# Kernel tuning notes

Measured on AMD Instinct MI355X. Metric: run time of the kernel, lower is better.

Reference implementation:

```python
import jax, jax.numpy as jnp
import numpy as np

DIM_V = 512
NUM_HEADS = 8
LN_EPS = 1e-5


def _layernorm(x):
    # LayerNorm over last dim, no affine (simplified_layer_norm=True)
    mu = jnp.mean(x, axis=-1, keepdims=True)
    var = jnp.mean(jnp.square(x - mu), axis=-1, keepdims=True)
    return (x - mu) * jax.lax.rsqrt(var + LN_EPS)


def setup_inputs() -> dict:
    key = jax.random.key(0)
    ks = jax.random.split(key, 12)
    B, Nq, Nk, dQ, dK, dV = 16, 1024, 1024, 512, 512, DIM_V
    s = 0.02
    return {
        "Q": jax.random.normal(ks[0], (B, Nq, dQ), jnp.float32),
        "K": jax.random.normal(ks[1], (B, Nk, dK), jnp.float32),
        "Wq": jax.random.normal(ks[2], (dQ, dV), jnp.float32) * s,
        "bq": jnp.zeros((dV,), jnp.float32),
        "Wk": jax.random.normal(ks[3], (dK, dV), jnp.float32) * s,
        "bk": jnp.zeros((dV,), jnp.float32),
        "Wv": jax.random.normal(ks[4], (dK, dV), jnp.float32) * s,
        "bv": jnp.zeros((dV,), jnp.float32),
        "Wo": jax.random.normal(ks[5], (dV, dV), jnp.float32) * s,
        "bo": jnp.zeros((dV,), jnp.float32),
    }


def reference(Q, K, Wq, bq, Wk, bk, Wv, bv, Wo, bo):
    H = NUM_HEADS
    dh = DIM_V // H
    q = Q @ Wq + bq            # [B, Nq, dV]
    k = K @ Wk + bk            # [B, Nk, dV]
    v = K @ Wv + bv            # [B, Nk, dV]
    B, Nq, _ = q.shape
    Nk = k.shape[1]
    qh = q.reshape(B, Nq, H, dh)
    kh = k.reshape(B, Nk, H, dh)
    vh = v.reshape(B, Nk, H, dh)
    # NOTE: faithful to source — scale by sqrt(dim_V), not sqrt(head_dim)
    scores = jnp.einsum('bqhd,bkhd->bhqk', qh, kh) / jnp.sqrt(jnp.asarray(DIM_V, q.dtype))
    A = jax.nn.softmax(scores, axis=-1)                    # [B, H, Nq, Nk]
    attn = jnp.einsum('bhqk,bkhd->bqhd', A, vh).reshape(B, Nq, DIM_V)
    O = q + attn               # residual with projected Q
    O = _layernorm(O)          # ln0 (no affine)
    O = O + jax.nn.gelu(O @ Wo + bo, approximate=False)
    O = _layernorm(O)          # ln1 (no affine)
    return O
```

## Files before the change

### kernel.cpp

```cpp
#include <hip/hip_runtime.h>
#include <hip/hip_bf16.h>
#include <math.h>

typedef __bf16 bf16;
typedef __bf16 bf16x8 __attribute__((ext_vector_type(8)));
typedef float  f32x4  __attribute__((ext_vector_type(4)));

#define MFMA16(a,b,c) __builtin_amdgcn_mfma_f32_16x16x32_bf16((a),(b),(c),0,0,0)
#define ATT_SCALE 0.0441941738241592f

__device__ __forceinline__ void async16p(const void* g, void* l) {
    __builtin_amdgcn_global_load_lds((const __attribute__((address_space(1))) void*)g,
                                     (__attribute__((address_space(3))) void*)l,
                                     16, 0, 0);
}

__global__ __launch_bounds__(256) void prep_w_kernel(
    const float* __restrict__ Wq, const float* __restrict__ Wk,
    const float* __restrict__ Wv, const float* __restrict__ Wo,
    bf16* __restrict__ WqT, bf16* __restrict__ WkT,
    bf16* __restrict__ WvT, bf16* __restrict__ WoT)
{
    __shared__ float tile[32][33];
    const int bx = blockIdx.x;
    const float* W; bf16* T;
    switch (bx >> 8) {
      case 0: W=Wq; T=WqT; break;
      case 1: W=Wk; T=WkT; break;
      case 2: W=Wv; T=WvT; break;
      default: W=Wo; T=WoT; break;
    }
    const int rest = bx & 255;
    const int k0 = (rest & 15) * 32, n0 = (rest >> 4) * 32;
    const int tx = threadIdx.x & 31, ty = threadIdx.x >> 5;
    #pragma unroll
    for (int i=0;i<32;i+=8)
        tile[ty+i][tx] = W[(size_t)(k0+ty+i)*512 + n0+tx];
    __syncthreads();
    #pragma unroll
    for (int i=0;i<32;i+=8)
        T[(size_t)(n0+ty+i)*512 + k0+tx] = (bf16)tile[tx][ty+i];
}

__global__ __launch_bounds__(256, 3) void gemm_qkv_kernel(
    const float* __restrict__ Qf, const float* __restrict__ Kf,
    const bf16* __restrict__ WqT, const bf16* __restrict__ WkT,
    const bf16* __restrict__ WvT,
    const float* __restrict__ bq, const float* __restrict__ bk,
    const float* __restrict__ bv,
    bf16* __restrict__ qbb, bf16* __restrict__ kbb, bf16* __restrict__ vT)
{
    __shared__ __align__(16) char smem[49152];
    float* As32 = (float*)smem;
    bf16*  Bs   = (bf16*)(smem + 32768);
    bf16*  Lt   = (bf16*)smem;

    const int z = blockIdx.z;
    const float* A  = (z == 0) ? Qf  : Kf;
    const bf16*  BT = (z == 0) ? WqT : (z == 1) ? WkT : WvT;
    const float* bb = (z == 0) ? bq  : (z == 1) ? bk  : bv;

    const int m0 = blockIdx.x * 128, n0 = blockIdx.y * 128;
    const int tid = threadIdx.x;
    const int lane = tid & 63, wave = tid >> 6;
    const int qd = lane >> 4, lr = lane & 15;
    const int wm = (wave & 1) * 64, wn = (wave >> 1) * 64;

    const float* gA = A + (size_t)(m0 + (tid>>3))*512 + (((tid&7)^((tid>>3)&7))*4);
    const bf16*  gB = BT + (size_t)(n0 + (tid>>2))*512 + (((tid&3)^((tid>>3)&3))*8);

    f32x4 acc[4][4];
    #pragma unroll
    for (int i=0;i<4;i++)
      #pragma unroll
      for (int j=0;j<4;j++) acc[i][j] = (f32x4){0,0,0,0};

    auto stage = [&](int buf, int k0) {
        float* lA = As32 + buf*4096 + wave*256;
        bf16*  lB = Bs   + buf*4096 + wave*512;
        #pragma unroll
        for (int i=0;i<4;i++)
            async16p(gA + k0 + (size_t)i*32*512, lA + i*1024);
        async16p(gB + k0,                  lB);
        async16p(gB + k0 + (size_t)64*512, lB + 2048);
    };

    stage(0, 0);
    for (int t = 0; t < 16; ++t) {
        const int cur = t & 1;
        __builtin_amdgcn_sched_barrier(0);
        __builtin_amdgcn_s_barrier();
        if (t < 15) {
            stage(cur ^ 1, (t+1)*32);
            asm volatile("s_waitcnt vmcnt(6)" ::: "memory");
        } else {
            asm volatile("s_waitcnt vmcnt(0)" ::: "memory");
        }
        __builtin_amdgcn_s_barrier();

        const float* Ab = As32 + cur*4096;
        const bf16*  Bb = Bs   + cur*4096;
        bf16x8 af[4], bfr[4];
        #pragma unroll
        for (int mi=0;mi<4;mi++) {
            int row = wm + mi*16 + lr;
            f32x4 f0 = *(f32x4*)(Ab + row*32 + (((qd*2  )^(lr&7))*4));
            f32x4 f1 = *(f32x4*)(Ab + row*32 + (((qd*2+1)^(lr&7))*4));
            bf16x8 a;
            a[0]=(bf16)f0[0]; a[1]=(bf16)f0[1]; a[2]=(bf16)f0[2]; a[3]=(bf16)f0[3];
            a[4]=(bf16)f1[0]; a[5]=(bf16)f1[1]; a[6]=(bf16)f1[2]; a[7]=(bf16)f1[3];
            af[mi] = a;
        }
        #pragma unroll
        for (int ni=0;ni<4;ni++)
            bfr[ni] = *(bf16x8*)(Bb + (wn+ni*16+lr)*32 + ((qd^((lr>>1)&3))*8));
        #pragma unroll
        for (int mi=0;mi<4;mi++)
          #pragma unroll
          for (int ni=0;ni<4;ni++)
            acc[mi][ni] = MFMA16(af[mi], bfr[ni], acc[mi][ni]);
    }

    if (z < 2) {
        bf16* C = (z == 0) ? qbb : kbb;
        #pragma unroll
        for (int ni=0;ni<4;ni++) {
            int n = n0 + wn + ni*16 + lr;
            float bv0 = bb[n];
            #pragma unroll
            for (int mi=0;mi<4;mi++) {
                int mb = m0 + wm + mi*16 + qd*4;
                #pragma unroll
                for (int r=0;r<4;r++)
                    C[(size_t)(mb+r)*512 + n] = (bf16)(acc[mi][ni][r] + bv0);
            }
        }
    } else {
        const int b = m0 >> 10, tok0 = m0 & 1023;
        const int row = tid >> 2, ch = tid & 3;
        #pragma unroll
        for (int half = 0; half < 2; ++half) {
            __syncthreads();
            if ((wn >> 6) == half) {
                #pragma unroll
                for (int ni=0;ni<4;ni++) {
                    int nl = ni*16 + lr;
                    float bvv = bb[n0 + half*64 + nl];
                    #pragma unroll
                    for (int mi=0;mi<4;mi++)
                      #pragma unroll
                      for (int r=0;r<4;r++) {
                        int col = wm + mi*16 + qd*4 + r;
                        Lt[nl*128 + ((((col>>3)^(nl&7))<<3) | (col&7))]
                            = (bf16)(acc[mi][ni][r] + bvv);
                      }
                }
            }
            __syncthreads();
            const int h = (n0 >> 6) + half;
            bf16* dst = vT + ((size_t)((b*8 + h)*64 + row))*1024 + tok0 + ch*32;
            #pragma unroll
            for (int s=0;s<4;s++) {
                int g = (ch*4 + s) ^ (row & 7);
                *(uint4*)(dst + s*8) = *(uint4*)(Lt + row*128 + g*8);
            }
        }
    }
}

__global__ __launch_bounds__(256, 4) void attn_kernel(
    const bf16* __restrict__ qb, const bf16* __restrict__ kb,
    const bf16* __restrict__ vT, bf16* __restrict__ attnb)
{
    const int qt = blockIdx.x, h = blockIdx.y, b = blockIdx.z;
    const int tid = threadIdx.x, lane = tid & 63, wave = tid >> 6;
    const int qd = lane >> 4, lr = lane & 15;
    const int q0 = qt*128 + wave*32;

    __shared__ bf16 Ks[64][72];
    __shared__ bf16 Vs[64][72];
    __shared__ bf16 Pl[4][32][72];

    bf16x8 aq[2][2];
    #pragma unroll
    for (int mi=0;mi<2;mi++) {
        const bf16* qrow = qb + ((size_t)(b*1024 + q0 + mi*16 + lr))*512 + h*64;
        aq[mi][0] = *(const bf16x8*)(qrow + qd*8);
        aq[mi][1] = *(const bf16x8*)(qrow + 32 + qd*8);
    }

    const int srow = tid >> 2;
    const int scol = (tid & 3) * 16;
    const bf16* kgp = kb + ((size_t)(b*1024 + srow))*512 + h*64 + scol;
    const bf16* vgp = vT + ((size_t)((b*8 + h)*64 + srow))*1024 + scol;

    uint4 k0r = *(const uint4*)(kgp);
    uint4 k1r = *(const uint4*)(kgp + 8);
    uint4 v0r = *(const uint4*)(vgp);
    uint4 v1r = *(const uint4*)(vgp + 8);

    f32x4 acc[2][4];
    #pragma unroll
    for (int mi=0;mi<2;mi++)
      #pragma unroll
      for (int ni=0;ni<4;ni++) acc[mi][ni] = (f32x4){0,0,0,0};
    float l[2][4] = {{0,0,0,0},{0,0,0,0}};

    for (int t=0; t<16; ++t) {
        __syncthreads();
        *(uint4*)(&Ks[srow][scol])   = k0r;
        *(uint4*)(&Ks[srow][scol+8]) = k1r;
        *(uint4*)(&Vs[srow][scol])   = v0r;
        *(uint4*)(&Vs[srow][scol+8]) = v1r;
        __syncthreads();
        if (t < 15) {
            const size_t kk = (size_t)(t+1)*64;
            k0r = *(const uint4*)(kgp + kk*512);
            k1r = *(const uint4*)(kgp + kk*512 + 8);
            v0r = *(const uint4*)(vgp + kk);
            v1r = *(const uint4*)(vgp + kk + 8);
        }

        f32x4 s[2][4];
        #pragma unroll
        for (int mi=0;mi<2;mi++)
          #pragma unroll
          for (int ni=0;ni<4;ni++) s[mi][ni] = (f32x4){0,0,0,0};
        #pragma unroll
        for (int ni=0;ni<4;ni++) {
            bf16x8 b0 = *(bf16x8*)(&Ks[ni*16+lr][qd*8]);
            bf16x8 b1 = *(bf16x8*)(&Ks[ni*16+lr][32+qd*8]);
            #pragma unroll
            for (int mi=0;mi<2;mi++) {
                s[mi][ni] = MFMA16(aq[mi][0], b0, s[mi][ni]);
                s[mi][ni] = MFMA16(aq[mi][1], b1, s[mi][ni]);
            }
        }
        #pragma unroll
        for (int mi=0;mi<2;mi++)
          #pragma unroll
          for (int ni=0;ni<4;ni++)
            #pragma unroll
            for (int r=0;r<4;r++) {
                float pv = __expf(s[mi][ni][r] * ATT_SCALE);
                s[mi][ni][r] = pv;
                l[mi][r] += pv;
            }
        #pragma unroll
        for (int mi=0;mi<2;mi++)
          #pragma unroll
          for (int ni=0;ni<4;ni++)
            #pragma unroll
            for (int r=0;r<4;r++)
                Pl[wave][mi*16 + qd*4 + r][ni*16 + lr] = (bf16)s[mi][ni][r];
        bf16x8 ap[2][2];
        #pragma unroll
        for (int mi=0;mi<2;mi++) {
            ap[mi][0] = *(bf16x8*)(&Pl[wave][mi*16+lr][qd*8]);
            ap[mi][1] = *(bf16x8*)(&Pl[wave][mi*16+lr][32+qd*8]);
        }
        #pragma unroll
        for (int ni=0;ni<4;ni++) {
            bf16x8 v0 = *(bf16x8*)(&Vs[ni*16+lr][qd*8]);
            bf16x8 v1 = *(bf16x8*)(&Vs[ni*16+lr][32+qd*8]);
            #pragma unroll
            for (int mi=0;mi<2;mi++) {
                acc[mi][ni] = MFMA16(ap[mi][0], v0, acc[mi][ni]);
                acc[mi][ni] = MFMA16(ap[mi][1], v1, acc[mi][ni]);
            }
        }
    }

    #pragma unroll
    for (int off=1; off<16; off<<=1)
      #pragma unroll
      for (int mi=0;mi<2;mi++)
        #pragma unroll
        for (int r=0;r<4;r++) l[mi][r] += __shfl_xor(l[mi][r], off);

    #pragma unroll
    for (int mi=0;mi<2;mi++) {
        float inv[4];
        #pragma unroll
        for (int r=0;r<4;r++) inv[r] = 1.f / l[mi][r];
        #pragma unroll
        for (int ni=0;ni<4;ni++)
          #pragma unroll
          for (int r=0;r<4;r++)
            Pl[wave][qd*4+r][ni*16+lr] = (bf16)(acc[mi][ni][r] * inv[r]);
        bf16x8 oA = *(bf16x8*)(&Pl[wave][lr][qd*8]);
        bf16x8 oB = *(bf16x8*)(&Pl[wave][lr][32+qd*8]);
        bf16x8 rA, rB;
        #pragma unroll
        for (int j=0;j<8;j++) {
            rA[j] = (bf16)((float)oA[j] + (float)aq[mi][0][j]);
            rB[j] = (bf16)((float)oB[j] + (float)aq[mi][1][j]);
        }
        bf16* dst = attnb + ((size_t)(b*1024 + q0 + mi*16 + lr))*512 + h*64;
        *(bf16x8*)(dst + qd*8)      = rA;
        *(bf16x8*)(dst + 32 + qd*8) = rB;
    }
}

__global__ __launch_bounds__(256) void ln0_kernel(
    const bf16* __restrict__ attnb, bf16* __restrict__ Obf)
{
    const int wave = threadIdx.x >> 6, lane = threadIdx.x & 63;
    const int row = blockIdx.x*4 + wave;
    const size_t base = (size_t)row*512 + lane*8;
    bf16x8 av = *(const bf16x8*)(attnb + base);
    float x[8];
    #pragma unroll
    for (int i=0;i<8;i++) x[i] = (float)av[i];
    float s1 = 0.f, s2 = 0.f;
    #pragma unroll
    for (int i=0;i<8;i++){ s1 += x[i]; s2 += x[i]*x[i]; }
    #pragma unroll
    for (int off=1; off<64; off<<=1) { s1 += __shfl_xor(s1, off); s2 += __shfl_xor(s2, off); }
    float mu  = s1 * (1.f/512.f);
    float var = s2 * (1.f/512.f) - mu*mu;
    float rstd = rsqrtf(var + 1e-5f);
    bf16x8 ob;
    #pragma unroll
    for (int i=0;i<8;i++) ob[i] = (bf16)((x[i]-mu)*rstd);
    *(bf16x8*)(Obf + base) = ob;
}

__device__ __forceinline__ void gemm_core(
    const bf16* __restrict__ A, const bf16* __restrict__ BT,
    int m0, int n0, char* smem, f32x4 (&acc)[4][4])
{
    bf16* As = (bf16*)smem;
    bf16* Bs = (bf16*)(smem + 16384);
    const int tid = threadIdx.x;
    const int lane = tid & 63, wave = tid >> 6;
    const int qd = lane >> 4, lr = lane & 15;
    const int wm = (wave & 1) * 64, wn = (wave >> 1) * 64;

    const int srow = tid >> 2;
    const int sgr  = ((tid & 3) ^ ((tid >> 3) & 3)) * 8;
    const bf16* gA = A  + (size_t)(m0 + srow)*512 + sgr;
    const bf16* gB = BT + (size_t)(n0 + srow)*512 + sgr;

    auto stage = [&](int buf, int k0) {
        bf16* lA = As + buf*4096 + wave*512;
        bf16* lB = Bs + buf*4096 + wave*512;
        async16p(gA + k0,                  lA);
        async16p(gA + k0 + (size_t)64*512, lA + 2048);
        async16p(gB + k0,                  lB);
        async16p(gB + k0 + (size_t)64*512, lB + 2048);
    };

    stage(0, 0);
    for (int t = 0; t < 16; ++t) {
        const int cur = t & 1;
        __builtin_amdgcn_sched_barrier(0);
        __builtin_amdgcn_s_barrier();
        if (t < 15) {
            stage(cur ^ 1, (t+1)*32);
            asm volatile("s_waitcnt vmcnt(4)" ::: "memory");
        } else {
            asm volatile("s_waitcnt vmcnt(0)" ::: "memory");
        }
        __builtin_amdgcn_s_barrier();

        const bf16* Ab = As + cur*4096;
        const bf16* Bb = Bs + cur*4096;
        bf16x8 af[4], bfr[4];
        #pragma unroll
        for (int mi=0;mi<4;mi++)
            af[mi] = *(bf16x8*)(Ab + (wm+mi*16+lr)*32 + ((qd^((lr>>1)&3))*8));
        #pragma unroll
        for (int ni=0;ni<4;ni++)
            bfr[ni] = *(bf16x8*)(Bb + (wn+ni*16+lr)*32 + ((qd^((lr>>1)&3))*8));
        #pragma unroll
        for (int mi=0;mi<4;mi++)
          #pragma unroll
          for (int ni=0;ni<4;ni++)
            acc[mi][ni] = MFMA16(af[mi], bfr[ni], acc[mi][ni]);
    }
}

__global__ __launch_bounds__(256, 4) void gemm_o_kernel(
    const bf16* __restrict__ Obf, const bf16* __restrict__ WoT,
    const float* __restrict__ bo, bf16* __restrict__ xb)
{
    __shared__ __align__(16) char smem[32768];
    const int m0 = blockIdx.x * 128, n0 = blockIdx.y * 128;
    const int tid = threadIdx.x;
    const int lane = tid & 63, wave = tid >> 6;
    const int qd = lane >> 4, lr = lane & 15;
    const int wm = (wave & 1) * 64, wn = (wave >> 1) * 64;

    f32x4 acc[4][4];
    #pragma unroll
    for (int i=0;i<4;i++)
      #pragma unroll
      for (int j=0;j<4;j++) acc[i][j] = (f32x4){0,0,0,0};

    gemm_core(Obf, WoT, m0, n0, smem, acc);

    #pragma unroll
    for (int ni=0;ni<4;ni++) {
        int n = n0 + wn + ni*16 + lr;
        float bv = bo[n];
        #pragma unroll
        for (int mi=0;mi<4;mi++) {
            int mb = m0 + wm + mi*16 + qd*4;
            #pragma unroll
            for (int r=0;r<4;r++) {
                float g = acc[mi][ni][r] + bv;
                float gelu = 0.5f * g * (1.f + erff(g * 0.70710678118654752f));
                size_t idx = (size_t)(mb+r)*512 + n;
                xb[idx] = (bf16)((float)Obf[idx] + gelu);
            }
        }
    }
}

__global__ __launch_bounds__(256) void ln1_kernel(
    const bf16* __restrict__ xb, float* __restrict__ out)
{
    const int wave = threadIdx.x >> 6, lane = threadIdx.x & 63;
    const int row = blockIdx.x*4 + wave;
    const size_t base = (size_t)row*512 + lane*8;
    bf16x8 xv = *(const bf16x8*)(xb + base);
    float x[8];
    #pragma unroll
    for (int i=0;i<8;i++) x[i] = (float)xv[i];
    float s1 = 0.f, s2 = 0.f;
    #pragma unroll
    for (int i=0;i<8;i++){ s1 += x[i]; s2 += x[i]*x[i]; }
    #pragma unroll
    for (int off=1; off<64; off<<=1) { s1 += __shfl_xor(s1, off); s2 += __shfl_xor(s2, off); }
    float mu  = s1 * (1.f/512.f);
    float var = s2 * (1.f/512.f) - mu*mu;
    float rstd = rsqrtf(var + 1e-5f);
    float4 o0 = {(x[0]-mu)*rstd,(x[1]-mu)*rstd,(x[2]-mu)*rstd,(x[3]-mu)*rstd};
    float4 o1 = {(x[4]-mu)*rstd,(x[5]-mu)*rstd,(x[6]-mu)*rstd,(x[7]-mu)*rstd};
    *(float4*)(out + base)     = o0;
    *(float4*)(out + base + 4) = o1;
}

extern "C" void kernel_launch(void* const* d_in, const int* in_sizes, int n_in,
                              void* d_out, int out_size, void* d_ws, size_t ws_size,
                              hipStream_t stream)
{
    (void)in_sizes; (void)n_in; (void)out_size; (void)ws_size;
    const float* Q  = (const float*)d_in[0];
    const float* K  = (const float*)d_in[1];
    const float* Wq = (const float*)d_in[2];
    const float* bq = (const float*)d_in[3];
    const float* Wk = (const float*)d_in[4];
    const float* bk = (const float*)d_in[5];
    const float* Wv = (const float*)d_in[6];
    const float* bv = (const float*)d_in[7];
    const float* Wo = (const float*)d_in[8];
    const float* bo = (const float*)d_in[9];
    float* out = (float*)d_out;

    const size_t nTok = (size_t)16*1024*512;
    char* p = (char*)d_ws;
    auto alloc = [&](size_t bytes)->char* {
        char* r = p; p += (bytes + 255) & ~(size_t)255; return r;
    };
    bf16* WqT   = (bf16*)alloc(512*512*2);
    bf16* WkT   = (bf16*)alloc(512*512*2);
    bf16* WvT   = (bf16*)alloc(512*512*2);
    bf16* WoT   = (bf16*)alloc(512*512*2);
    bf16* qbb   = (bf16*)alloc(nTok*2);
    bf16* kbb   = (bf16*)alloc(nTok*2);
    bf16* vT    = (bf16*)alloc(nTok*2);
    bf16* attnb = (bf16*)alloc(nTok*2);
    bf16* Obf   = (bf16*)alloc(nTok*2);
    bf16* xb    = (bf16*)alloc(nTok*2);

    prep_w_kernel<<<1024, 256, 0, stream>>>(Wq, Wk, Wv, Wo, WqT, WkT, WvT, WoT);
    gemm_qkv_kernel<<<dim3(128,4,3), 256, 0, stream>>>(Q, K, WqT, WkT, WvT,
                                                       bq, bk, bv, qbb, kbb, vT);
    attn_kernel<<<dim3(8,8,16), 256, 0, stream>>>(qbb, kbb, vT, attnb);
    ln0_kernel<<<4096, 256, 0, stream>>>(attnb, Obf);
    gemm_o_kernel<<<dim3(128,4), 256, 0, stream>>>(Obf, WoT, bo, xb);
    ln1_kernel<<<4096, 256, 0, stream>>>(xb, out);
}
```

Before: 268.1 us.

## Rewrite attention kernel with 32x32 MFMA, async LDS double buffering, register-resident P

The attention kernel now uses 32x32x16 bf16 MFMAs and computes S transposed, so the exponentiated probabilities can be repacked in registers via permlane32 swaps instead of round-tripping through shared memory. K/V tiles are loaded with global_load_lds into a double-buffered, XOR-swizzled LDS buffer, with waitcnt-based pipelining in place of register staging and two full syncthreads per tile. The grid is flattened so that consecutive blocks share the same batch's K/V, improving L2 reuse. The epilogue writes outputs with scalar bf16 stores plus a residual read, which may be less coalesced than before.

```diff
diff --git a/kernel.cpp b/kernel.cpp
--- a/kernel.cpp
+++ b/kernel.cpp
@@ -5,14 +5,36 @@
 typedef __bf16 bf16;
 typedef __bf16 bf16x8 __attribute__((ext_vector_type(8)));
 typedef float  f32x4  __attribute__((ext_vector_type(4)));
+typedef float  f32x16 __attribute__((ext_vector_type(16)));
+typedef unsigned u32x4 __attribute__((ext_vector_type(4)));
 
 #define MFMA16(a,b,c) __builtin_amdgcn_mfma_f32_16x16x32_bf16((a),(b),(c),0,0,0)
+#define MFMA32(a,b,c) __builtin_amdgcn_mfma_f32_32x32x16_bf16((a),(b),(c),0,0,0)
 #define ATT_SCALE 0.0441941738241592f
 
 __device__ __forceinline__ void async16p(const void* g, void* l) {
     __builtin_amdgcn_global_load_lds((const __attribute__((address_space(1))) void*)g,
                                      (__attribute__((address_space(3))) void*)l,
                                      16, 0, 0);
+}
+
+__device__ __forceinline__ unsigned pkbf(float a, float b) {
+    union { bf16 h[2]; unsigned u; } x;
+    x.h[0] = (bf16)a; x.h[1] = (bf16)b; return x.u;
+}
+
+__device__ __forceinline__ void plswap(unsigned &a, unsigned &b) {
+#if __has_builtin(__builtin_amdgcn_permlane32_swap)
+    auto r = __builtin_amdgcn_permlane32_swap((int)a, (int)b, false, false);
+    a = (unsigned)r[0]; b = (unsigned)r[1];
+#else
+    unsigned sa = (unsigned)__shfl_xor((int)a, 32);
+    unsigned sb = (unsigned)__shfl_xor((int)b, 32);
+    bool hi = (threadIdx.x & 32) != 0;
+    unsigned na = hi ? sb : a;
+    unsigned nb = hi ? b  : sa;
+    a = na; b = nb;
+#endif
 }
 
 __global__ __launch_bounds__(256) void prep_w_kernel(
@@ -172,133 +194,117 @@
     const bf16* __restrict__ qb, const bf16* __restrict__ kb,
     const bf16* __restrict__ vT, bf16* __restrict__ attnb)
 {
-    const int qt = blockIdx.x, h = blockIdx.y, b = blockIdx.z;
+    const int x = blockIdx.x;
+    const int qt = x >> 7, h = x & 7, b = (x & 127) >> 3;
     const int tid = threadIdx.x, lane = tid & 63, wave = tid >> 6;
-    const int qd = lane >> 4, lr = lane & 15;
-    const int q0 = qt*128 + wave*32;
-
-    __shared__ bf16 Ks[64][72];
-    __shared__ bf16 Vs[64][72];
-    __shared__ bf16 Pl[4][32][72];
-
-    bf16x8 aq[2][2];
-    #pragma unroll
-    for (int mi=0;mi<2;mi++) {
-        const bf16* qrow = qb + ((size_t)(b*1024 + q0 + mi*16 + lr))*512 + h*64;
-        aq[mi][0] = *(const bf16x8*)(qrow + qd*8);
-        aq[mi][1] = *(const bf16x8*)(qrow + 32 + qd*8);
-    }
-
-    const int srow = tid >> 2;
-    const int scol = (tid & 3) * 16;
-    const bf16* kgp = kb + ((size_t)(b*1024 + srow))*512 + h*64 + scol;
-    const bf16* vgp = vT + ((size_t)((b*8 + h)*64 + srow))*1024 + scol;
-
-    uint4 k0r = *(const uint4*)(kgp);
-    uint4 k1r = *(const uint4*)(kgp + 8);
-    uint4 v0r = *(const uint4*)(vgp);
-    uint4 v1r = *(const uint4*)(vgp + 8);
-
-    f32x4 acc[2][4];
-    #pragma unroll
-    for (int mi=0;mi<2;mi++)
-      #pragma unroll
-      for (int ni=0;ni<4;ni++) acc[mi][ni] = (f32x4){0,0,0,0};
-    float l[2][4] = {{0,0,0,0},{0,0,0,0}};
-
+    const int l = lane & 31, hi = lane >> 5;
+    const int q0w = qt*128 + wave*32;
+
+    __shared__ __align__(16) bf16 kv[2][2][4096];
+    __shared__ float ls[4][32];
+
+    bf16x8 aq[4];
+    {
+        const bf16* qrow = qb + ((size_t)(b*1024 + q0w + l))*512 + h*64 + hi*8;
+        #pragma unroll
+        for (int st=0; st<4; ++st) aq[st] = *(const bf16x8*)(qrow + st*16);
+    }
+
+    const int srow = lane >> 3;
+    const int sg   = (lane & 7) ^ srow;
+    const bf16* kg0 = kb + ((size_t)(b*1024 + wave*8 + srow))*512 + h*64 + sg*8;
+    const bf16* vg0 = vT + ((size_t)((b*8 + h)*64 + wave*8 + srow))*1024 + sg*8;
+
+    auto stage = [&](int buf, int t) {
+        const size_t ko = (size_t)t*64*512;
+        async16p(kg0 + ko,                   &kv[buf][0][wave*512]);
+        async16p(kg0 + ko + (size_t)32*512,  &kv[buf][0][2048 + wave*512]);
+        async16p(vg0 + t*64,                 &kv[buf][1][wave*512]);
+        async16p(vg0 + t*64 + 32*1024,       &kv[buf][1][2048 + wave*512]);
+    };
+
+    f32x16 accO[2];
+    accO[0] = (f32x16)0.f; accO[1] = (f32x16)0.f;
+    float lsum = 0.f;
+
+    stage(0, 0);
     for (int t=0; t<16; ++t) {
-        __syncthreads();
-        *(uint4*)(&Ks[srow][scol])   = k0r;
-        *(uint4*)(&Ks[srow][scol+8]) = k1r;
-        *(uint4*)(&Vs[srow][scol])   = v0r;
-        *(uint4*)(&Vs[srow][scol+8]) = v1r;
-        __syncthreads();
+        const int cur = t & 1;
+        __builtin_amdgcn_sched_barrier(0);
+        __builtin_amdgcn_s_barrier();
         if (t < 15) {
-            const size_t kk = (size_t)(t+1)*64;
-            k0r = *(const uint4*)(kgp + kk*512);
-            k1r = *(const uint4*)(kgp + kk*512 + 8);
-            v0r = *(const uint4*)(vgp + kk);
-            v1r = *(const uint4*)(vgp + kk + 8);
-        }
-
-        f32x4 s[2][4];
-        #pragma unroll
-        for (int mi=0;mi<2;mi++)
-          #pragma unroll
-          for (int ni=0;ni<4;ni++) s[mi][ni] = (f32x4){0,0,0,0};
-        #pragma unroll
-        for (int ni=0;ni<4;ni++) {
-            bf16x8 b0 = *(bf16x8*)(&Ks[ni*16+lr][qd*8]);
-            bf16x8 b1 = *(bf16x8*)(&Ks[ni*16+lr][32+qd*8]);
-            #pragma unroll
-            for (int mi=0;mi<2;mi++) {
-                s[mi][ni] = MFMA16(aq[mi][0], b0, s[mi][ni]);
-                s[mi][ni] = MFMA16(aq[mi][1], b1, s[mi][ni]);
-            }
-        }
-        #pragma unroll
-        for (int mi=0;mi<2;mi++)
-          #pragma unroll
-          for (int ni=0;ni<4;ni++)
-            #pragma unroll
-            for (int r=0;r<4;r++) {
-                float pv = __expf(s[mi][ni][r] * ATT_SCALE);
-                s[mi][ni][r] = pv;
-                l[mi][r] += pv;
-            }
-        #pragma unroll
-        for (int mi=0;mi<2;mi++)
-          #pragma unroll
-          for (int ni=0;ni<4;ni++)
-            #pragma unroll
-            for (int r=0;r<4;r++)
-                Pl[wave][mi*16 + qd*4 + r][ni*16 + lr] = (bf16)s[mi][ni][r];
-        bf16x8 ap[2][2];
-        #pragma unroll
-        for (int mi=0;mi<2;mi++) {
-            ap[mi][0] = *(bf16x8*)(&Pl[wave][mi*16+lr][qd*8]);
-            ap[mi][1] = *(bf16x8*)(&Pl[wave][mi*16+lr][32+qd*8]);
-        }
-        #pragma unroll
-        for (int ni=0;ni<4;ni++) {
-            bf16x8 v0 = *(bf16x8*)(&Vs[ni*16+lr][qd*8]);
-            bf16x8 v1 = *(bf16x8*)(&Vs[ni*16+lr][32+qd*8]);
-            #pragma unroll
-            for (int mi=0;mi<2;mi++) {
-                acc[mi][ni] = MFMA16(ap[mi][0], v0, acc[mi][ni]);
-                acc[mi][ni] = MFMA16(ap[mi][1], v1, acc[mi][ni]);
-            }
-        }
-    }
-
-    #pragma unroll
-    for (int off=1; off<16; off<<=1)
-      #pragma unroll
-      for (int mi=0;mi<2;mi++)
-        #pragma unroll
-        for (int r=0;r<4;r++) l[mi][r] += __shfl_xor(l[mi][r], off);
-
-    #pragma unroll
-    for (int mi=0;mi<2;mi++) {
-        float inv[4];
-        #pragma unroll
-        for (int r=0;r<4;r++) inv[r] = 1.f / l[mi][r];
-        #pragma unroll
-        for (int ni=0;ni<4;ni++)
-          #pragma unroll
-          for (int r=0;r<4;r++)
-            Pl[wave][qd*4+r][ni*16+lr] = (bf16)(acc[mi][ni][r] * inv[r]);
-        bf16x8 oA = *(bf16x8*)(&Pl[wave][lr][qd*8]);
-        bf16x8 oB = *(bf16x8*)(&Pl[wave][lr][32+qd*8]);
-        bf16x8 rA, rB;
-        #pragma unroll
-        for (int j=0;j<8;j++) {
-            rA[j] = (bf16)((float)oA[j] + (float)aq[mi][0][j]);
-            rB[j] = (bf16)((float)oB[j] + (float)aq[mi][1][j]);
-        }
-        bf16* dst = attnb + ((size_t)(b*1024 + q0 + mi*16 + lr))*512 + h*64;
-        *(bf16x8*)(dst + qd*8)      = rA;
-        *(bf16x8*)(dst + 32 + qd*8) = rB;
+            stage(cur ^ 1, t + 1);
+            asm volatile("s_waitcnt vmcnt(4)" ::: "memory");
+        } else {
+            asm volatile("s_waitcnt vmcnt(0)" ::: "memory");
+        }
+        __builtin_amdgcn_s_barrier();
+
+        const bf16* Ks = kv[cur][0];
+        const bf16* Vs = kv[cur][1];
+
+        u32x4 paf[4];
+        #pragma unroll
+        for (int kb2=0; kb2<2; ++kb2) {
+            f32x16 sT = (f32x16)0.f;
+            #pragma unroll
+            for (int st=0; st<4; ++st) {
+                bf16x8 kf = *(const bf16x8*)(Ks + (kb2*32 + l)*64
+                                               + (((st*2 + hi) ^ (l & 7))*8));
+                sT = MFMA32(kf, aq[st], sT);
+            }
+            unsigned u[8];
+            #pragma unroll
+            for (int m=0; m<8; ++m) {
+                float e0 = __expf(sT[2*m]   * ATT_SCALE);
+                float e1 = __expf(sT[2*m+1] * ATT_SCALE);
+                lsum += e0 + e1;
+                u[m] = pkbf(e0, e1);
+            }
+            #pragma unroll
+            for (int sb=0; sb<2; ++sb) {
+                unsigned a0=u[4*sb], a1=u[4*sb+1], a2=u[4*sb+2], a3=u[4*sb+3];
+                plswap(a0, a2);
+                plswap(a1, a3);
+                paf[kb2*2 + sb] = (u32x4){a0, a1, a2, a3};
+            }
+        }
+        #pragma unroll
+        for (int db=0; db<2; ++db) {
+            f32x16 a = accO[db];
+            #pragma unroll
+            for (int st=0; st<4; ++st) {
+                bf16x8 vf = *(const bf16x8*)(Vs + (db*32 + l)*64
+                                               + (((st*2 + hi) ^ (l & 7))*8));
+                u32x4 pp = paf[st];
+                bf16x8 pf = *(bf16x8*)&pp;
+                a = MFMA32(pf, vf, a);
+            }
+            accO[db] = a;
+        }
+    }
+
+    lsum += __shfl_xor(lsum, 32);
+    ls[wave][l] = lsum;
+    __syncthreads();
+
+    #pragma unroll
+    for (int g=0; g<4; ++g) {
+        f32x4 lv = *(const f32x4*)(&ls[wave][g*8 + hi*4]);
+        f32x4 inv;
+        #pragma unroll
+        for (int i=0;i<4;i++) inv[i] = 1.f / lv[i];
+        #pragma unroll
+        for (int db=0; db<2; ++db) {
+            #pragma unroll
+            for (int i=0;i<4;i++) {
+                int r = g*4 + i;
+                int qrow = q0w + g*8 + hi*4 + i;
+                size_t idx = ((size_t)(b*1024 + qrow))*512 + h*64 + db*32 + l;
+                float o = accO[db][r] * inv[i] + (float)qb[idx];
+                attnb[idx] = (bf16)o;
+            }
+        }
     }
 }
 
@@ -478,7 +484,7 @@
     prep_w_kernel<<<1024, 256, 0, stream>>>(Wq, Wk, Wv, Wo, WqT, WkT, WvT, WoT);
     gemm_qkv_kernel<<<dim3(128,4,3), 256, 0, stream>>>(Q, K, WqT, WkT, WvT,
                                                        bq, bk, bv, qbb, kbb, vT);
-    attn_kernel<<<dim3(8,8,16), 256, 0, stream>>>(qbb, kbb, vT, attnb);
+    attn_kernel<<<dim3(1024), 256, 0, stream>>>(qbb, kbb, vT, attnb);
     ln0_kernel<<<4096, 256, 0, stream>>>(attnb, Obf);
     gemm_o_kernel<<<dim3(128,4), 256, 0, stream>>>(Obf, WoT, bo, xb);
     ln1_kernel<<<4096, 256, 0, stream>>>(xb, out);
```

Result: faster. 257.4 us (-4.0%).
